# Kernel tuning notes

Measured on AMD Instinct MI355X. Metric: run time of the kernel, lower is better.

The kernel has to match this reference:

```python
import jax, jax.numpy as jnp
import numpy as np

D_MODEL = 1024
NUM_HEADS = 16
D_K = D_MODEL // NUM_HEADS


def setup_inputs() -> dict:
    key = jax.random.key(0)
    ks = jax.random.split(key, 9)
    B, S = 2, 2048
    s = 1.0 / np.sqrt(D_MODEL)
    inp = {
        "x": jax.random.normal(ks[0], (B, S, D_MODEL), dtype=jnp.float32),
        "Wq": jax.random.normal(ks[1], (D_MODEL, D_MODEL), dtype=jnp.float32) * s,
        "bq": jnp.zeros((D_MODEL,), dtype=jnp.float32),
        "Wk": jax.random.normal(ks[2], (D_MODEL, D_MODEL), dtype=jnp.float32) * s,
        "bk": jnp.zeros((D_MODEL,), dtype=jnp.float32),
        "Wv": jax.random.normal(ks[3], (D_MODEL, D_MODEL), dtype=jnp.float32) * s,
        "bv": jnp.zeros((D_MODEL,), dtype=jnp.float32),
        "Wo": jax.random.normal(ks[4], (D_MODEL, D_MODEL), dtype=jnp.float32) * s,
        "bo": jnpp if False else jnp.zeros((D_MODEL,), dtype=jnp.float32),
    }
    return inp


def reference(x, Wq, bq, Wk, bk, Wv, bv, Wo, bo):
    B, S, _ = x.shape
    H, Dk = NUM_HEADS, D_K

    def proj(W, b):
        # [B,S,D] -> [B,H,S,Dk]
        return (x @ W + b).reshape(B, S, H, Dk).transpose(0, 2, 1, 3)

    Q = proj(Wq, bq)
    K = proj(Wk, bk)
    V = proj(Wv, bv)

    scores = jnp.einsum("bhqd,bhkd->bhqk", Q, K) / np.sqrt(Dk)
    attn = jax.nn.softmax(scores, axis=-1)  # no mask, dropout p=0 (eval)
    out = jnp.einsum("bhqk,bhkd->bhqd", attn, V)
    out = out.transpose(0, 2, 1, 3).reshape(B, S, D_MODEL)
    return out @ Wo + bo
```

## Files before the change

kernel.cpp:

```cpp
#include <hip/hip_runtime.h>
#include <hip/hip_bf16.h>
#include <cstdint>
#include <math.h>

#define D_MODEL 1024
#define NHEADS  16
#define DK      64
#define BATCH   2
#define SEQ     2048
#define M_TOTAL (BATCH*SEQ)

using f32x4  = __attribute__((ext_vector_type(4)))  float;
using f32x16 = __attribute__((ext_vector_type(16))) float;
using s16x8  = __attribute__((ext_vector_type(8)))  short;

#define CSC (0.125f * 1.44269504088896341f)

__device__ __forceinline__ unsigned short bf16r(float f) {
    __hip_bfloat16 h = __float2bfloat16(f);
    return *(unsigned short*)&h;
}
__device__ __forceinline__ uint32_t packbf(float lo, float hi) {
    return (uint32_t)bf16r(lo) | ((uint32_t)bf16r(hi) << 16);
}

__global__ __launch_bounds__(256) void conv_x(const float* __restrict__ x,
                                              unsigned short* __restrict__ xb)
{
    const size_t i = ((size_t)blockIdx.x * 256 + threadIdx.x) * 8;
    const float4 a = *(const float4*)(x + i);
    const float4 b = *(const float4*)(x + i + 4);
    ushort4 r0, r1;
    r0.x = bf16r(a.x); r0.y = bf16r(a.y); r0.z = bf16r(a.z); r0.w = bf16r(a.w);
    r1.x = bf16r(b.x); r1.y = bf16r(b.y); r1.z = bf16r(b.z); r1.w = bf16r(b.w);
    *(ushort4*)(xb + i)     = r0;
    *(ushort4*)(xb + i + 4) = r1;
}

__global__ __launch_bounds__(256) void conv_wt(const float* __restrict__ W0, const float* __restrict__ W1,
                                               const float* __restrict__ W2, const float* __restrict__ W3,
                                               unsigned short* __restrict__ T0, unsigned short* __restrict__ T1,
                                               unsigned short* __restrict__ T2, unsigned short* __restrict__ T3)
{
    const float* W; unsigned short* T;
    switch (blockIdx.z) {
        case 0: W = W0; T = T0; break;
        case 1: W = W1; T = T1; break;
        case 2: W = W2; T = T2; break;
        default: W = W3; T = T3; break;
    }
    __shared__ float tile[32][33];
    const int t  = threadIdx.x;
    const int r  = t >> 3;
    const int c4 = (t & 7) * 4;
    const int k0 = blockIdx.x * 32;
    const int n0 = blockIdx.y * 32;

    const float4 v = *(const float4*)(W + (size_t)(k0 + r) * 1024 + n0 + c4);
    tile[r][c4 + 0] = v.x; tile[r][c4 + 1] = v.y; tile[r][c4 + 2] = v.z; tile[r][c4 + 3] = v.w;
    __syncthreads();
    ushort4 o;
    o.x = bf16r(tile[c4 + 0][r]);
    o.y = bf16r(tile[c4 + 1][r]);
    o.z = bf16r(tile[c4 + 2][r]);
    o.w = bf16r(tile[c4 + 3][r]);
    *(ushort4*)(T + (size_t)(n0 + r) * 1024 + k0 + c4) = o;
}

template<int OUT_BF16>
__device__ __forceinline__ void gemm_mfma_body(const unsigned short* __restrict__ A,
                                               const unsigned short* __restrict__ Bt,
                                               const float* __restrict__ bias,
                                               void* __restrict__ C,
                                               float oscale)
{
    __shared__ unsigned short As[128 * 64];
    __shared__ unsigned short Bs[128 * 64];

    const int t    = threadIdx.x;
    const int w    = t >> 6;
    const int lane = t & 63;
    const int ln   = lane & 15;
    const int g    = lane >> 4;
    const int wr   = w >> 1, wc = w & 1;
    const int m0   = blockIdx.y * 128;
    const int n0   = blockIdx.x * 128;

    f32x4 acc[4][4];
#pragma unroll
    for (int mi = 0; mi < 4; ++mi)
#pragma unroll
        for (int ni = 0; ni < 4; ++ni)
#pragma unroll
            for (int j = 0; j < 4; ++j) acc[mi][ni][j] = 0.f;

    const int lrow = lane >> 3;
    const int lchk = (lane & 7) ^ lrow;
    const unsigned short* Ag = A  + (size_t)(m0 + w * 32 + lrow) * 1024 + lchk * 8;
    const unsigned short* Bg = Bt + (size_t)(n0 + w * 32 + lrow) * 1024 + lchk * 8;

    for (int kt = 0; kt < 16; ++kt) {
        const int k0 = kt * 64;
#pragma unroll
        for (int i = 0; i < 4; ++i) {
            __builtin_amdgcn_global_load_lds(Ag + (size_t)i * 8 * 1024 + k0,
                                             &As[(w * 32 + i * 8) * 64], 16, 0, 0);
            __builtin_amdgcn_global_load_lds(Bg + (size_t)i * 8 * 1024 + k0,
                                             &Bs[(w * 32 + i * 8) * 64], 16, 0, 0);
        }
        __syncthreads();

#pragma unroll
        for (int ks = 0; ks < 2; ++ks) {
            s16x8 af[4], bf[4];
#pragma unroll
            for (int mi = 0; mi < 4; ++mi) {
                const int row = wr * 64 + mi * 16 + ln;
                af[mi] = *(const s16x8*)((const char*)As + row * 128 +
                                         (((ks * 4 + g) ^ (ln & 7)) * 16));
            }
#pragma unroll
            for (int ni = 0; ni < 4; ++ni) {
                const int row = wc * 64 + ni * 16 + ln;
                bf[ni] = *(const s16x8*)((const char*)Bs + row * 128 +
                                         (((ks * 4 + g) ^ (ln & 7)) * 16));
            }
#pragma unroll
            for (int mi = 0; mi < 4; ++mi)
#pragma unroll
                for (int ni = 0; ni < 4; ++ni)
                    acc[mi][ni] = __builtin_amdgcn_mfma_f32_16x16x32_bf16(
                        af[mi], bf[ni], acc[mi][ni], 0, 0, 0);
        }
        __syncthreads();
    }

#pragma unroll
    for (int ni = 0; ni < 4; ++ni) {
        const int n = n0 + wc * 64 + ni * 16 + ln;
        const float bn = bias[n];
#pragma unroll
        for (int mi = 0; mi < 4; ++mi) {
            const int m = m0 + wr * 64 + mi * 16 + g * 4;
#pragma unroll
            for (int j = 0; j < 4; ++j) {
                const float v = (acc[mi][ni][j] + bn) * oscale;
                if constexpr (OUT_BF16)
                    ((unsigned short*)C)[(size_t)(m + j) * 1024 + n] = bf16r(v);
                else
                    ((float*)C)[(size_t)(m + j) * 1024 + n] = v;
            }
        }
    }
}

__global__ __launch_bounds__(256) void qkv_mfma(const unsigned short* __restrict__ xb,
                                                const unsigned short* __restrict__ Wqt, const float* __restrict__ bq,
                                                const unsigned short* __restrict__ Wkt, const float* __restrict__ bk,
                                                const unsigned short* __restrict__ Wvt, const float* __restrict__ bv,
                                                unsigned short* __restrict__ Q,
                                                unsigned short* __restrict__ K,
                                                unsigned short* __restrict__ V)
{
    const unsigned short* Bt; const float* bias; unsigned short* C; float sc;
    if (blockIdx.z == 0)      { Bt = Wqt; bias = bq; C = Q; sc = CSC; }
    else if (blockIdx.z == 1) { Bt = Wkt; bias = bk; C = K; sc = 1.0f; }
    else                      { Bt = Wvt; bias = bv; C = V; sc = 1.0f; }
    gemm_mfma_body<1>(xb, Bt, bias, C, sc);
}

__global__ __launch_bounds__(256) void oproj_mfma(const unsigned short* __restrict__ Ab,
                                                  const unsigned short* __restrict__ Wot,
                                                  const float* __restrict__ bo,
                                                  float* __restrict__ C)
{
    gemm_mfma_body<0>(Ab, Wot, bo, C, 1.0f);
}

__global__ __launch_bounds__(256, 2) void attn_mfma(const unsigned short* __restrict__ Qb,
                                                    const unsigned short* __restrict__ Kb,
                                                    const unsigned short* __restrict__ Vb,
                                                    unsigned short* __restrict__ O)
{
    __shared__ unsigned short Klds [64 * 64];
    __shared__ unsigned short Vtlds[64 * 64];

    const int t   = threadIdx.x;
    const int wid = t >> 6;
    const int l   = t & 63;
    const int q32 = l & 31;
    const int hi  = l >> 5;

    const int bh = blockIdx.y;
    const int b  = bh >> 4;
    const int h  = bh & 15;
    const int qbase = blockIdx.x * 128 + wid * 32;
    const size_t qrow = (size_t)(b * SEQ + qbase + q32);
    const size_t kv0  = (size_t)(b * SEQ);

    s16x8 qf[4];
    {
        const unsigned short* qp = Qb + qrow * D_MODEL + h * DK + 8 * hi;
        qf[0] = *(const s16x8*)(qp);
        qf[1] = *(const s16x8*)(qp + 16);
        qf[2] = *(const s16x8*)(qp + 32);
        qf[3] = *(const s16x8*)(qp + 48);
    }

    f32x16 ot0, ot1;
#pragma unroll
    for (int i = 0; i < 16; ++i) { ot0[i] = 0.f; ot1[i] = 0.f; }
    float mrun = -INFINITY, lsum = 0.f;

    const int skey = t >> 3;
    const int sc8  = t & 7;
    const int vk2  = 2 * (t & 31);
    const int vd0  = 8 * (t >> 5);
    const unsigned short* Kg = Kb + (kv0 + skey) * D_MODEL + h * DK + 8 * sc8;
    const unsigned short* Vg = Vb + (kv0 + vk2) * D_MODEL + h * DK + vd0;
    char* const kw0 = (char*)Klds + skey * 128        + 16 * (sc8 ^ (skey & 7));
    char* const kw1 = (char*)Klds + (skey + 32) * 128 + 16 * (sc8 ^ (skey & 7));

    s16x8 kr0, kr1, vr0, vr1;

    auto write_stage = [&]() {
        *(s16x8*)kw0 = kr0;
        *(s16x8*)kw1 = kr1;
#pragma unroll
        for (int i = 0; i < 8; ++i) {
            const int d = vd0 + i;
            const uint32_t val = (uint32_t)(unsigned short)vr0[i] |
                                 ((uint32_t)(unsigned short)vr1[i] << 16);
            *(uint32_t*)((char*)Vtlds + d * 128 + 16 * ((vk2 >> 3) ^ (d & 7)) + (vk2 & 7) * 2) = val;
        }
    };

    kr0 = *(const s16x8*)(Kg);
    kr1 = *(const s16x8*)(Kg + (size_t)32 * D_MODEL);
    vr0 = *(const s16x8*)(Vg);
    vr1 = *(const s16x8*)(Vg + D_MODEL);
    write_stage();
    __syncthreads();

    for (int kt = 0; kt < SEQ / 64; ++kt) {
        if (kt < SEQ / 64 - 1) {
            const size_t off = (size_t)(kt + 1) * 64 * D_MODEL;
            kr0 = *(const s16x8*)(Kg + off);
            kr1 = *(const s16x8*)(Kg + off + (size_t)32 * D_MODEL);
            vr0 = *(const s16x8*)(Vg + off);
            vr1 = *(const s16x8*)(Vg + off + D_MODEL);
        }

        f32x16 s0, s1;
#pragma unroll
        for (int i = 0; i < 16; ++i) { s0[i] = 0.f; s1[i] = 0.f; }
#pragma unroll
        for (int ks = 0; ks < 4; ++ks) {
            const int c = hi + 2 * ks;
            const s16x8 a0 = *(const s16x8*)((char*)Klds + q32 * 128 +
                                             16 * (c ^ (q32 & 7)));
            const s16x8 a1 = *(const s16x8*)((char*)Klds + (q32 + 32) * 128 +
                                             16 * (c ^ (q32 & 7)));
            s0 = __builtin_amdgcn_mfma_f32_32x32x16_bf16(a0, qf[ks], s0, 0, 0, 0);
            s1 = __builtin_amdgcn_mfma_f32_32x32x16_bf16(a1, qf[ks], s1, 0, 0, 0);
        }

        float mc = s0[0];
#pragma unroll
        for (int i = 1; i < 16; ++i) mc = fmaxf(mc, s0[i]);
#pragma unroll
        for (int i = 0; i < 16; ++i) mc = fmaxf(mc, s1[i]);
        mc = fmaxf(mc, __shfl_xor(mc, 32));

        if (!__all(mc - mrun <= 8.0f)) {
            const float mnew = fmaxf(mrun, mc);
            const float r = exp2f(mrun - mnew);
            lsum *= r;
#pragma unroll
            for (int i = 0; i < 16; ++i) { ot0[i] *= r; ot1[i] *= r; }
            mrun = mnew;
        }

        float ls = 0.f;
#pragma unroll
        for (int i = 0; i < 16; ++i) {
            s0[i] = exp2f(s0[i] - mrun); ls += s0[i];
            s1[i] = exp2f(s1[i] - mrun); ls += s1[i];
        }
        lsum += ls;

        s16x8 pf[4];
#pragma unroll
        for (int half = 0; half < 2; ++half) {
            const f32x16& sv = half ? s1 : s0;
            uint32_t W[8], Y[8];
#pragma unroll
            for (int j = 0; j < 8; ++j) W[j] = packbf(sv[2 * j], sv[2 * j + 1]);
#pragma unroll
            for (int j = 0; j < 8; ++j) Y[j] = __shfl_xor(W[j], 32);
            union { uint32_t u[4]; s16x8 v; } F0, F1;
            F0.u[0] = hi ? Y[2] : W[0];
            F0.u[1] = hi ? Y[3] : W[1];
            F0.u[2] = hi ? W[2] : Y[0];
            F0.u[3] = hi ? W[3] : Y[1];
            F1.u[0] = hi ? Y[6] : W[4];
            F1.u[1] = hi ? Y[7] : W[5];
            F1.u[2] = hi ? W[6] : Y[4];
            F1.u[3] = hi ? W[7] : Y[5];
            pf[2 * half]     = F0.v;
            pf[2 * half + 1] = F1.v;
        }

#pragma unroll
        for (int ks = 0; ks < 4; ++ks) {
            const int c = hi + 2 * ks;
            const s16x8 av0 = *(const s16x8*)((char*)Vtlds + q32 * 128 +
                                              16 * (c ^ (q32 & 7)));
            const s16x8 av1 = *(const s16x8*)((char*)Vtlds + (q32 + 32) * 128 +
                                              16 * (c ^ (q32 & 7)));
            ot0 = __builtin_amdgcn_mfma_f32_32x32x16_bf16(av0, pf[ks], ot0, 0, 0, 0);
            ot1 = __builtin_amdgcn_mfma_f32_32x32x16_bf16(av1, pf[ks], ot1, 0, 0, 0);
        }

        __syncthreads();
        if (kt < SEQ / 64 - 1) write_stage();
        __syncthreads();
    }

    const float inv = 1.0f / (lsum + __shfl_xor(lsum, 32));
    unsigned short* op = O + qrow * D_MODEL + h * DK;
#pragma unroll
    for (int j = 0; j < 4; ++j) {
        ushort4 st0, st1;
        st0.x = bf16r(ot0[4 * j + 0] * inv);
        st0.y = bf16r(ot0[4 * j + 1] * inv);
        st0.z = bf16r(ot0[4 * j + 2] * inv);
        st0.w = bf16r(ot0[4 * j + 3] * inv);
        st1.x = bf16r(ot1[4 * j + 0] * inv);
        st1.y = bf16r(ot1[4 * j + 1] * inv);
        st1.z = bf16r(ot1[4 * j + 2] * inv);
        st1.w = bf16r(ot1[4 * j + 3] * inv);
        *(ushort4*)(op + 8 * j + 4 * hi)      = st0;
        *(ushort4*)(op + 32 + 8 * j + 4 * hi) = st1;
    }
}

extern "C" void kernel_launch(void* const* d_in, const int* in_sizes, int n_in,
                              void* d_out, int out_size, void* d_ws, size_t ws_size,
                              hipStream_t stream)
{
    const float* x  = (const float*)d_in[0];
    const float* Wq = (const float*)d_in[1];
    const float* bq = (const float*)d_in[2];
    const float* Wk = (const float*)d_in[3];
    const float* bk = (const float*)d_in[4];
    const float* Wv = (const float*)d_in[5];
    const float* bv = (const float*)d_in[6];
    const float* Wo = (const float*)d_in[7];
    const float* bo = (const float*)d_in[8];

    float* out = (float*)d_out;

    const size_t mat  = (size_t)M_TOTAL * D_MODEL;
    const size_t wmat = (size_t)D_MODEL * D_MODEL;
    unsigned short* xb  = (unsigned short*)d_ws;
    unsigned short* Wqt = xb  + mat;
    unsigned short* Wkt = Wqt + wmat;
    unsigned short* Wvt = Wkt + wmat;
    unsigned short* Wot = Wvt + wmat;
    unsigned short* Qb  = Wot + wmat;
    unsigned short* Kb  = Qb  + mat;
    unsigned short* Vb  = Kb  + mat;
    unsigned short* Ab  = Vb  + mat;

    conv_x<<<dim3(2048), 256, 0, stream>>>(x, xb);
    conv_wt<<<dim3(32, 32, 4), 256, 0, stream>>>(Wq, Wk, Wv, Wo, Wqt, Wkt, Wvt, Wot);

    qkv_mfma<<<dim3(8, 32, 3), 256, 0, stream>>>(xb, Wqt, bq, Wkt, bk, Wvt, bv, Qb, Kb, Vb);

    attn_mfma<<<dim3(SEQ / 128, BATCH * NHEADS), 256, 0, stream>>>(Qb, Kb, Vb, Ab);

    oproj_mfma<<<dim3(8, 32), 256, 0, stream>>>(Ab, Wot, bo, out);
}
```

Measured before the change: 155.5 us.

## Write V transposed from QKV GEMM and load K/V fragments directly into registers

The V projection epilogue now writes V transposed ([D, B*S]), so the attention kernel can load V operand fragments straight from global memory. K and V fragments are register-prefetched one tile ahead, and the shared-memory staging and both per-tile __syncthreads barriers are removed. The row-max and exp-sum reductions are also split into four independent chains to shorten dependencies. The cost is that each wave now fetches the same K/V tiles separately from global memory or L2, with no sharing through LDS, and register pressure rises from the 16 fragment registers.

```diff
diff --git a/kernel.cpp b/kernel.cpp
--- a/kernel.cpp
+++ b/kernel.cpp
@@ -9,6 +9,7 @@
 #define BATCH   2
 #define SEQ     2048
 #define M_TOTAL (BATCH*SEQ)
+#define NT      (SEQ/64)
 
 using f32x4  = __attribute__((ext_vector_type(4)))  float;
 using f32x16 = __attribute__((ext_vector_type(16))) float;
@@ -67,7 +68,7 @@
     *(ushort4*)(T + (size_t)(n0 + r) * 1024 + k0 + c4) = o;
 }
 
-template<int OUT_BF16>
+template<int MODE>
 __device__ __forceinline__ void gemm_mfma_body(const unsigned short* __restrict__ A,
                                                const unsigned short* __restrict__ Bt,
                                                const float* __restrict__ bias,
@@ -142,13 +143,22 @@
 #pragma unroll
         for (int mi = 0; mi < 4; ++mi) {
             const int m = m0 + wr * 64 + mi * 16 + g * 4;
-#pragma unroll
-            for (int j = 0; j < 4; ++j) {
-                const float v = (acc[mi][ni][j] + bn) * oscale;
-                if constexpr (OUT_BF16)
-                    ((unsigned short*)C)[(size_t)(m + j) * 1024 + n] = bf16r(v);
-                else
-                    ((float*)C)[(size_t)(m + j) * 1024 + n] = v;
+            if constexpr (MODE == 2) {
+                ushort4 pk;
+                pk.x = bf16r((acc[mi][ni][0] + bn) * oscale);
+                pk.y = bf16r((acc[mi][ni][1] + bn) * oscale);
+                pk.z = bf16r((acc[mi][ni][2] + bn) * oscale);
+                pk.w = bf16r((acc[mi][ni][3] + bn) * oscale);
+                *(ushort4*)((unsigned short*)C + (size_t)n * 4096 + m) = pk;
+            } else {
+#pragma unroll
+                for (int j = 0; j < 4; ++j) {
+                    const float v = (acc[mi][ni][j] + bn) * oscale;
+                    if constexpr (MODE == 1)
+                        ((unsigned short*)C)[(size_t)(m + j) * 1024 + n] = bf16r(v);
+                    else
+                        ((float*)C)[(size_t)(m + j) * 1024 + n] = v;
+                }
             }
         }
     }
@@ -160,13 +170,11 @@
                                                 const unsigned short* __restrict__ Wvt, const float* __restrict__ bv,
                                                 unsigned short* __restrict__ Q,
                                                 unsigned short* __restrict__ K,
-                                                unsigned short* __restrict__ V)
-{
-    const unsigned short* Bt; const float* bias; unsigned short* C; float sc;
-    if (blockIdx.z == 0)      { Bt = Wqt; bias = bq; C = Q; sc = CSC; }
-    else if (blockIdx.z == 1) { Bt = Wkt; bias = bk; C = K; sc = 1.0f; }
-    else                      { Bt = Wvt; bias = bv; C = V; sc = 1.0f; }
-    gemm_mfma_body<1>(xb, Bt, bias, C, sc);
+                                                unsigned short* __restrict__ Vt)
+{
+    if (blockIdx.z == 0)      gemm_mfma_body<1>(xb, Wqt, bq, Q,  CSC);
+    else if (blockIdx.z == 1) gemm_mfma_body<1>(xb, Wkt, bk, K,  1.0f);
+    else                      gemm_mfma_body<2>(xb, Wvt, bv, Vt, 1.0f);
 }
 
 __global__ __launch_bounds__(256) void oproj_mfma(const unsigned short* __restrict__ Ab,
@@ -179,12 +187,9 @@
 
 __global__ __launch_bounds__(256, 2) void attn_mfma(const unsigned short* __restrict__ Qb,
                                                     const unsigned short* __restrict__ Kb,
-                                                    const unsigned short* __restrict__ Vb,
+                                                    const unsigned short* __restrict__ Vt,
                                                     unsigned short* __restrict__ O)
 {
-    __shared__ unsigned short Klds [64 * 64];
-    __shared__ unsigned short Vtlds[64 * 64];
-
     const int t   = threadIdx.x;
     const int wid = t >> 6;
     const int l   = t & 63;
@@ -201,10 +206,22 @@
     s16x8 qf[4];
     {
         const unsigned short* qp = Qb + qrow * D_MODEL + h * DK + 8 * hi;
-        qf[0] = *(const s16x8*)(qp);
-        qf[1] = *(const s16x8*)(qp + 16);
-        qf[2] = *(const s16x8*)(qp + 32);
-        qf[3] = *(const s16x8*)(qp + 48);
+#pragma unroll
+        for (int ks = 0; ks < 4; ++ks) qf[ks] = *(const s16x8*)(qp + 16 * ks);
+    }
+
+    const unsigned short* KA = Kb + (kv0 + q32) * D_MODEL + h * DK + 8 * hi;
+    const unsigned short* KB = KA + (size_t)32 * D_MODEL;
+    const unsigned short* VA = Vt + (size_t)(h * DK + q32) * 4096 + b * SEQ + 8 * hi;
+    const unsigned short* VB = VA + (size_t)32 * 4096;
+
+    s16x8 kf[8], vf[8];
+#pragma unroll
+    for (int ks = 0; ks < 4; ++ks) {
+        kf[ks]     = *(const s16x8*)(KA + 16 * ks);
+        kf[4 + ks] = *(const s16x8*)(KB + 16 * ks);
+        vf[ks]     = *(const s16x8*)(VA + 16 * ks);
+        vf[4 + ks] = *(const s16x8*)(VB + 16 * ks);
     }
 
     f32x16 ot0, ot1;
@@ -212,64 +229,38 @@
     for (int i = 0; i < 16; ++i) { ot0[i] = 0.f; ot1[i] = 0.f; }
     float mrun = -INFINITY, lsum = 0.f;
 
-    const int skey = t >> 3;
-    const int sc8  = t & 7;
-    const int vk2  = 2 * (t & 31);
-    const int vd0  = 8 * (t >> 5);
-    const unsigned short* Kg = Kb + (kv0 + skey) * D_MODEL + h * DK + 8 * sc8;
-    const unsigned short* Vg = Vb + (kv0 + vk2) * D_MODEL + h * DK + vd0;
-    char* const kw0 = (char*)Klds + skey * 128        + 16 * (sc8 ^ (skey & 7));
-    char* const kw1 = (char*)Klds + (skey + 32) * 128 + 16 * (sc8 ^ (skey & 7));
-
-    s16x8 kr0, kr1, vr0, vr1;
-
-    auto write_stage = [&]() {
-        *(s16x8*)kw0 = kr0;
-        *(s16x8*)kw1 = kr1;
-#pragma unroll
-        for (int i = 0; i < 8; ++i) {
-            const int d = vd0 + i;
-            const uint32_t val = (uint32_t)(unsigned short)vr0[i] |
-                                 ((uint32_t)(unsigned short)vr1[i] << 16);
-            *(uint32_t*)((char*)Vtlds + d * 128 + 16 * ((vk2 >> 3) ^ (d & 7)) + (vk2 & 7) * 2) = val;
-        }
-    };
-
-    kr0 = *(const s16x8*)(Kg);
-    kr1 = *(const s16x8*)(Kg + (size_t)32 * D_MODEL);
-    vr0 = *(const s16x8*)(Vg);
-    vr1 = *(const s16x8*)(Vg + D_MODEL);
-    write_stage();
-    __syncthreads();
-
-    for (int kt = 0; kt < SEQ / 64; ++kt) {
-        if (kt < SEQ / 64 - 1) {
-            const size_t off = (size_t)(kt + 1) * 64 * D_MODEL;
-            kr0 = *(const s16x8*)(Kg + off);
-            kr1 = *(const s16x8*)(Kg + off + (size_t)32 * D_MODEL);
-            vr0 = *(const s16x8*)(Vg + off);
-            vr1 = *(const s16x8*)(Vg + off + D_MODEL);
-        }
-
+    for (int kt = 0; kt < NT; ++kt) {
         f32x16 s0, s1;
 #pragma unroll
         for (int i = 0; i < 16; ++i) { s0[i] = 0.f; s1[i] = 0.f; }
 #pragma unroll
         for (int ks = 0; ks < 4; ++ks) {
-            const int c = hi + 2 * ks;
-            const s16x8 a0 = *(const s16x8*)((char*)Klds + q32 * 128 +
-                                             16 * (c ^ (q32 & 7)));
-            const s16x8 a1 = *(const s16x8*)((char*)Klds + (q32 + 32) * 128 +
-                                             16 * (c ^ (q32 & 7)));
-            s0 = __builtin_amdgcn_mfma_f32_32x32x16_bf16(a0, qf[ks], s0, 0, 0, 0);
-            s1 = __builtin_amdgcn_mfma_f32_32x32x16_bf16(a1, qf[ks], s1, 0, 0, 0);
-        }
-
-        float mc = s0[0];
-#pragma unroll
-        for (int i = 1; i < 16; ++i) mc = fmaxf(mc, s0[i]);
-#pragma unroll
-        for (int i = 0; i < 16; ++i) mc = fmaxf(mc, s1[i]);
+            s0 = __builtin_amdgcn_mfma_f32_32x32x16_bf16(kf[ks],     qf[ks], s0, 0, 0, 0);
+            s1 = __builtin_amdgcn_mfma_f32_32x32x16_bf16(kf[4 + ks], qf[ks], s1, 0, 0, 0);
+        }
+
+        const int ktn = (kt + 1 < NT) ? kt + 1 : NT - 1;
+        {
+            const size_t ko = (size_t)ktn * 64 * D_MODEL;
+#pragma unroll
+            for (int ks = 0; ks < 4; ++ks) {
+                kf[ks]     = *(const s16x8*)(KA + ko + 16 * ks);
+                kf[4 + ks] = *(const s16x8*)(KB + ko + 16 * ks);
+            }
+        }
+
+        float c0 = s0[0], c1 = s0[1], c2 = s0[2], c3 = s0[3];
+#pragma unroll
+        for (int i = 1; i < 4; ++i) {
+            c0 = fmaxf(c0, s0[4 * i + 0]); c1 = fmaxf(c1, s0[4 * i + 1]);
+            c2 = fmaxf(c2, s0[4 * i + 2]); c3 = fmaxf(c3, s0[4 * i + 3]);
+        }
+#pragma unroll
+        for (int i = 0; i < 4; ++i) {
+            c0 = fmaxf(c0, s1[4 * i + 0]); c1 = fmaxf(c1, s1[4 * i + 1]);
+            c2 = fmaxf(c2, s1[4 * i + 2]); c3 = fmaxf(c3, s1[4 * i + 3]);
+        }
+        float mc = fmaxf(fmaxf(c0, c1), fmaxf(c2, c3));
         mc = fmaxf(mc, __shfl_xor(mc, 32));
 
         if (!__all(mc - mrun <= 8.0f)) {
@@ -281,13 +272,19 @@
             mrun = mnew;
         }
 
-        float ls = 0.f;
-#pragma unroll
-        for (int i = 0; i < 16; ++i) {
-            s0[i] = exp2f(s0[i] - mrun); ls += s0[i];
-            s1[i] = exp2f(s1[i] - mrun); ls += s1[i];
-        }
-        lsum += ls;
+        float l0 = 0.f, l1 = 0.f, l2 = 0.f, l3 = 0.f;
+#pragma unroll
+        for (int i = 0; i < 4; ++i) {
+            s0[4 * i + 0] = exp2f(s0[4 * i + 0] - mrun); l0 += s0[4 * i + 0];
+            s0[4 * i + 1] = exp2f(s0[4 * i + 1] - mrun); l1 += s0[4 * i + 1];
+            s0[4 * i + 2] = exp2f(s0[4 * i + 2] - mrun); l2 += s0[4 * i + 2];
+            s0[4 * i + 3] = exp2f(s0[4 * i + 3] - mrun); l3 += s0[4 * i + 3];
+            s1[4 * i + 0] = exp2f(s1[4 * i + 0] - mrun); l0 += s1[4 * i + 0];
+            s1[4 * i + 1] = exp2f(s1[4 * i + 1] - mrun); l1 += s1[4 * i + 1];
+            s1[4 * i + 2] = exp2f(s1[4 * i + 2] - mrun); l2 += s1[4 * i + 2];
+            s1[4 * i + 3] = exp2f(s1[4 * i + 3] - mrun); l3 += s1[4 * i + 3];
+        }
+        lsum += (l0 + l1) + (l2 + l3);
 
         s16x8 pf[4];
 #pragma unroll
@@ -313,18 +310,18 @@
 
 #pragma unroll
         for (int ks = 0; ks < 4; ++ks) {
-            const int c = hi + 2 * ks;
-            const s16x8 av0 = *(const s16x8*)((char*)Vtlds + q32 * 128 +
-                                              16 * (c ^ (q32 & 7)));
-            const s16x8 av1 = *(const s16x8*)((char*)Vtlds + (q32 + 32) * 128 +
-                                              16 * (c ^ (q32 & 7)));
-            ot0 = __builtin_amdgcn_mfma_f32_32x32x16_bf16(av0, pf[ks], ot0, 0, 0, 0);
-            ot1 = __builtin_amdgcn_mfma_f32_32x32x16_bf16(av1, pf[ks], ot1, 0, 0, 0);
-        }
-
-        __syncthreads();
-        if (kt < SEQ / 64 - 1) write_stage();
-        __syncthreads();
+            ot0 = __builtin_amdgcn_mfma_f32_32x32x16_bf16(vf[ks],     pf[ks], ot0, 0, 0, 0);
+            ot1 = __builtin_amdgcn_mfma_f32_32x32x16_bf16(vf[4 + ks], pf[ks], ot1, 0, 0, 0);
+        }
+
+        {
+            const size_t vo = (size_t)ktn * 64;
+#pragma unroll
+            for (int ks = 0; ks < 4; ++ks) {
+                vf[ks]     = *(const s16x8*)(VA + vo + 16 * ks);
+                vf[4 + ks] = *(const s16x8*)(VB + vo + 16 * ks);
+            }
+        }
     }
 
     const float inv = 1.0f / (lsum + __shfl_xor(lsum, 32));
@@ -370,15 +367,15 @@
     unsigned short* Wot = Wvt + wmat;
     unsigned short* Qb  = Wot + wmat;
     unsigned short* Kb  = Qb  + mat;
-    unsigned short* Vb  = Kb  + mat;
-    unsigned short* Ab  = Vb  + mat;
+    unsigned short* Vt  = Kb  + mat;
+    unsigned short* Ab  = Vt  + mat;
 
     conv_x<<<dim3(2048), 256, 0, stream>>>(x, xb);
     conv_wt<<<dim3(32, 32, 4), 256, 0, stream>>>(Wq, Wk, Wv, Wo, Wqt, Wkt, Wvt, Wot);
 
-    qkv_mfma<<<dim3(8, 32, 3), 256, 0, stream>>>(xb, Wqt, bq, Wkt, bk, Wvt, bv, Qb, Kb, Vb);
-
-    attn_mfma<<<dim3(SEQ / 128, BATCH * NHEADS), 256, 0, stream>>>(Qb, Kb, Vb, Ab);
+    qkv_mfma<<<dim3(8, 32, 3), 256, 0, stream>>>(xb, Wqt, bq, Wkt, bk, Wvt, bv, Qb, Kb, Vt);
+
+    attn_mfma<<<dim3(SEQ / 128, BATCH * NHEADS), 256, 0, stream>>>(Qb, Kb, Vt, Ab);
 
     oproj_mfma<<<dim3(8, 32), 256, 0, stream>>>(Ab, Wot, bo, out);
 }
```

Result: slower. 202.0 us (+29.9%).

## Split attention KV range across two blocks and merge partials in combine kernel

Applied to the files above, without the earlier changes.

The attention kernel gains a third grid dimension that splits the 2048-key sequence into two halves. Each half writes an unnormalised bf16 partial output plus its running max and sum, and a new combine kernel rescales and merges them into the final attention buffer. The aim is more blocks in flight and shorter per-block loops, in exchange for an extra launch and a write-then-read of the partials. The bf16 packing in the softmax and in the store path also switches to the v_cvt_pk_bf16_f32 instruction to cut VALU work.

```diff
diff --git a/kernel.cpp b/kernel.cpp
--- a/kernel.cpp
+++ b/kernel.cpp
@@ -9,6 +9,8 @@
 #define BATCH   2
 #define SEQ     2048
 #define M_TOTAL (BATCH*SEQ)
+#define NSPLIT  2
+#define NTS     (SEQ/64/NSPLIT)
 
 using f32x4  = __attribute__((ext_vector_type(4)))  float;
 using f32x16 = __attribute__((ext_vector_type(16))) float;
@@ -20,8 +22,16 @@
     __hip_bfloat16 h = __float2bfloat16(f);
     return *(unsigned short*)&h;
 }
-__device__ __forceinline__ uint32_t packbf(float lo, float hi) {
-    return (uint32_t)bf16r(lo) | ((uint32_t)bf16r(hi) << 16);
+__device__ __forceinline__ uint32_t cvtpk(float lo, float hi) {
+    uint32_t r;
+    asm("v_cvt_pk_bf16_f32 %0, %1, %2" : "=v"(r) : "v"(lo), "v"(hi));
+    return r;
+}
+__device__ __forceinline__ float b2f(unsigned short u) {
+    uint32_t x = (uint32_t)u << 16;
+    float f;
+    __builtin_memcpy(&f, &x, 4);
+    return f;
 }
 
 __global__ __launch_bounds__(256) void conv_x(const float* __restrict__ x,
@@ -162,11 +172,9 @@
                                                 unsigned short* __restrict__ K,
                                                 unsigned short* __restrict__ V)
 {
-    const unsigned short* Bt; const float* bias; unsigned short* C; float sc;
-    if (blockIdx.z == 0)      { Bt = Wqt; bias = bq; C = Q; sc = CSC; }
-    else if (blockIdx.z == 1) { Bt = Wkt; bias = bk; C = K; sc = 1.0f; }
-    else                      { Bt = Wvt; bias = bv; C = V; sc = 1.0f; }
-    gemm_mfma_body<1>(xb, Bt, bias, C, sc);
+    if (blockIdx.z == 0)      gemm_mfma_body<1>(xb, Wqt, bq, Q, CSC);
+    else if (blockIdx.z == 1) gemm_mfma_body<1>(xb, Wkt, bk, K, 1.0f);
+    else                      gemm_mfma_body<1>(xb, Wvt, bv, V, 1.0f);
 }
 
 __global__ __launch_bounds__(256) void oproj_mfma(const unsigned short* __restrict__ Ab,
@@ -180,7 +188,8 @@
 __global__ __launch_bounds__(256, 2) void attn_mfma(const unsigned short* __restrict__ Qb,
                                                     const unsigned short* __restrict__ Kb,
                                                     const unsigned short* __restrict__ Vb,
-                                                    unsigned short* __restrict__ O)
+                                                    unsigned short* __restrict__ Opart,
+                                                    float2* __restrict__ ml)
 {
     __shared__ unsigned short Klds [64 * 64];
     __shared__ unsigned short Vtlds[64 * 64];
@@ -194,17 +203,16 @@
     const int bh = blockIdx.y;
     const int b  = bh >> 4;
     const int h  = bh & 15;
+    const int sp = blockIdx.z;
     const int qbase = blockIdx.x * 128 + wid * 32;
     const size_t qrow = (size_t)(b * SEQ + qbase + q32);
-    const size_t kv0  = (size_t)(b * SEQ);
+    const size_t kv0  = (size_t)(b * SEQ) + (size_t)sp * (SEQ / NSPLIT);
 
     s16x8 qf[4];
     {
         const unsigned short* qp = Qb + qrow * D_MODEL + h * DK + 8 * hi;
-        qf[0] = *(const s16x8*)(qp);
-        qf[1] = *(const s16x8*)(qp + 16);
-        qf[2] = *(const s16x8*)(qp + 32);
-        qf[3] = *(const s16x8*)(qp + 48);
+#pragma unroll
+        for (int ks = 0; ks < 4; ++ks) qf[ks] = *(const s16x8*)(qp + 16 * ks);
     }
 
     f32x16 ot0, ot1;
@@ -242,8 +250,8 @@
     write_stage();
     __syncthreads();
 
-    for (int kt = 0; kt < SEQ / 64; ++kt) {
-        if (kt < SEQ / 64 - 1) {
+    for (int kt = 0; kt < NTS; ++kt) {
+        if (kt < NTS - 1) {
             const size_t off = (size_t)(kt + 1) * 64 * D_MODEL;
             kr0 = *(const s16x8*)(Kg + off);
             kr1 = *(const s16x8*)(Kg + off + (size_t)32 * D_MODEL);
@@ -295,7 +303,7 @@
             const f32x16& sv = half ? s1 : s0;
             uint32_t W[8], Y[8];
 #pragma unroll
-            for (int j = 0; j < 8; ++j) W[j] = packbf(sv[2 * j], sv[2 * j + 1]);
+            for (int j = 0; j < 8; ++j) W[j] = cvtpk(sv[2 * j], sv[2 * j + 1]);
 #pragma unroll
             for (int j = 0; j < 8; ++j) Y[j] = __shfl_xor(W[j], 32);
             union { uint32_t u[4]; s16x8 v; } F0, F1;
@@ -323,26 +331,66 @@
         }
 
         __syncthreads();
-        if (kt < SEQ / 64 - 1) write_stage();
+        if (kt < NTS - 1) write_stage();
         __syncthreads();
     }
 
-    const float inv = 1.0f / (lsum + __shfl_xor(lsum, 32));
-    unsigned short* op = O + qrow * D_MODEL + h * DK;
+    const float ltot = lsum + __shfl_xor(lsum, 32);
+    const size_t prow = (size_t)bh * SEQ + qbase + q32;
+    if (hi == 0)
+        ml[(size_t)sp * (BATCH * NHEADS * SEQ) + prow] = make_float2(mrun, ltot);
+
+    unsigned short* op = Opart + (size_t)sp * ((size_t)BATCH * NHEADS * SEQ * DK)
+                               + prow * DK;
 #pragma unroll
     for (int j = 0; j < 4; ++j) {
-        ushort4 st0, st1;
-        st0.x = bf16r(ot0[4 * j + 0] * inv);
-        st0.y = bf16r(ot0[4 * j + 1] * inv);
-        st0.z = bf16r(ot0[4 * j + 2] * inv);
-        st0.w = bf16r(ot0[4 * j + 3] * inv);
-        st1.x = bf16r(ot1[4 * j + 0] * inv);
-        st1.y = bf16r(ot1[4 * j + 1] * inv);
-        st1.z = bf16r(ot1[4 * j + 2] * inv);
-        st1.w = bf16r(ot1[4 * j + 3] * inv);
-        *(ushort4*)(op + 8 * j + 4 * hi)      = st0;
-        *(ushort4*)(op + 32 + 8 * j + 4 * hi) = st1;
-    }
+        uint2 st0, st1;
+        st0.x = cvtpk(ot0[4 * j + 0], ot0[4 * j + 1]);
+        st0.y = cvtpk(ot0[4 * j + 2], ot0[4 * j + 3]);
+        st1.x = cvtpk(ot1[4 * j + 0], ot1[4 * j + 1]);
+        st1.y = cvtpk(ot1[4 * j + 2], ot1[4 * j + 3]);
+        *(uint2*)(op + 8 * j + 4 * hi)      = st0;
+        *(uint2*)(op + 32 + 8 * j + 4 * hi) = st1;
+    }
+}
+
+__global__ __launch_bounds__(256) void attn_combine(const unsigned short* __restrict__ Opart,
+                                                    const float2* __restrict__ ml,
+                                                    unsigned short* __restrict__ Ab)
+{
+    const int tid = blockIdx.x * 256 + threadIdx.x;
+    const int row = tid >> 3;
+    const int d0  = (tid & 7) * 8;
+    const size_t NROW = (size_t)BATCH * NHEADS * SEQ;
+
+    const float2 a = ml[row];
+    const float2 c = ml[NROW + row];
+    const float mm = fmaxf(a.x, c.x);
+    const float w0 = exp2f(a.x - mm);
+    const float w1 = exp2f(c.x - mm);
+    const float rinv = 1.0f / (w0 * a.y + w1 * c.y);
+
+    const size_t src = (size_t)row * DK + d0;
+    const ushort4 u0 = *(const ushort4*)(Opart + src);
+    const ushort4 u1 = *(const ushort4*)(Opart + src + 4);
+    const ushort4 v0 = *(const ushort4*)(Opart + NROW * DK + src);
+    const ushort4 v1 = *(const ushort4*)(Opart + NROW * DK + src + 4);
+
+    const int bh = row >> 11, s = row & 2047;
+    const int b = bh >> 4, h = bh & 15;
+    unsigned short* dst = Ab + ((size_t)(b * SEQ + s)) * D_MODEL + h * DK + d0;
+
+    ushort4 o0, o1;
+    o0.x = bf16r((w0 * b2f(u0.x) + w1 * b2f(v0.x)) * rinv);
+    o0.y = bf16r((w0 * b2f(u0.y) + w1 * b2f(v0.y)) * rinv);
+    o0.z = bf16r((w0 * b2f(u0.z) + w1 * b2f(v0.z)) * rinv);
+    o0.w = bf16r((w0 * b2f(u0.w) + w1 * b2f(v0.w)) * rinv);
+    o1.x = bf16r((w0 * b2f(u1.x) + w1 * b2f(v1.x)) * rinv);
+    o1.y = bf16r((w0 * b2f(u1.y) + w1 * b2f(v1.y)) * rinv);
+    o1.z = bf16r((w0 * b2f(u1.z) + w1 * b2f(v1.z)) * rinv);
+    o1.w = bf16r((w0 * b2f(u1.w) + w1 * b2f(v1.w)) * rinv);
+    *(ushort4*)(dst)     = o0;
+    *(ushort4*)(dst + 4) = o1;
 }
 
 extern "C" void kernel_launch(void* const* d_in, const int* in_sizes, int n_in,
@@ -372,13 +420,17 @@
     unsigned short* Kb  = Qb  + mat;
     unsigned short* Vb  = Kb  + mat;
     unsigned short* Ab  = Vb  + mat;
+    unsigned short* Op  = Ab  + mat;
+    float2*         ml  = (float2*)d_ws;
 
     conv_x<<<dim3(2048), 256, 0, stream>>>(x, xb);
     conv_wt<<<dim3(32, 32, 4), 256, 0, stream>>>(Wq, Wk, Wv, Wo, Wqt, Wkt, Wvt, Wot);
 
     qkv_mfma<<<dim3(8, 32, 3), 256, 0, stream>>>(xb, Wqt, bq, Wkt, bk, Wvt, bv, Qb, Kb, Vb);
 
-    attn_mfma<<<dim3(SEQ / 128, BATCH * NHEADS), 256, 0, stream>>>(Qb, Kb, Vb, Ab);
+    attn_mfma<<<dim3(SEQ / 128, BATCH * NHEADS, NSPLIT), 256, 0, stream>>>(Qb, Kb, Vb, Op, ml);
+
+    attn_combine<<<dim3((BATCH * NHEADS * SEQ * 8) / 256), 256, 0, stream>>>(Op, ml, Ab);
 
     oproj_mfma<<<dim3(8, 32), 256, 0, stream>>>(Ab, Wot, bo, out);
 }
```

New measurement: 151.5 us. 1.03x faster.
